# Performance work log

Hardware: AMD Instinct MI355X
Metric: run time of the kernel (lower is better)

## Reference

```python
import jax, jax.numpy as jnp
import numpy as np

B, N_FRAMES, C, S = 4, 32, 256, 16
D = 512            # attn_dim = min(C*S*S, 512)
NHEADS = 8
TOKEN = C * S * S  # 65536
EPS = 1e-5


def _layer_norm_last(x, g, b):
    mu = x.mean(-1, keepdims=True)
    var = x.var(-1, keepdims=True)
    return (x - mu) * jax.lax.rsqrt(var + EPS) * g + b


def _forward(feat, Wp, bp, Wu, bu, Wq, bq, Wk, bk, Wv, bv, Wo, bo, ln1_g, ln1_b,
             Wk1, bk1, Wk2, bk2, Wpc, bpc, gn_g, gn_b, Wf1, bf1, Wf2, bf2,
             dn_g, dn_b, num_frames):
    BN, Cc, H, W = feat.shape
    N = num_frames
    Bb = BN // N
    # 1) flatten frames to tokens and project (B, N, token_dim) -> (B, N, D)
    tokens = feat.reshape(Bb, N, Cc * H * W)
    tp = tokens @ Wp.T + bp
    # contextual grouping with clamped indices: K = v_{n-1}, Q = v_n, V = v_{n+1}
    idx = jnp.arange(N)
    v_prev = tp[:, jnp.maximum(idx - 1, 0)]
    v_next = tp[:, jnp.minimum(idx + 1, N - 1)]
    # 2) MHA with seq_len 1 for Q/K/V (degenerate softmax over a single key)
    dh = D // NHEADS
    q = (tp @ Wq.T + bq).reshape(Bb, N, NHEADS, dh)
    k = (v_prev @ Wk.T + bk).reshape(Bb, N, NHEADS, dh)
    v = (v_next @ Wv.T + bv).reshape(Bb, N, NHEADS, dh)
    scores = jnp.sum(q * k, axis=-1, keepdims=True) / jnp.sqrt(jnp.float32(dh))  # (B,N,h,1)
    wts = jax.nn.softmax(scores, axis=-1)  # identically 1.0 (single key)
    attn = (wts * v).reshape(Bb, N, D) @ Wo.T + bo
    enh = _layer_norm_last(attn + tp, ln1_g, ln1_b)
    # 3) unproject back to feature maps
    feat_attn = (enh @ Wu.T + bu).reshape(BN, Cc, H, W)
    # 4) DynamicConv: per-sample depthwise 3x3 kernels conditioned on GAP
    gap = feat_attn.mean((2, 3))                       # (BN, C)
    hid = jax.nn.relu(gap @ Wk1.T + bk1)
    kern = (hid @ Wk2.T + bk2).reshape(BN, Cc, 3, 3)   # per-sample, per-channel kernels
    xp = jnp.pad(feat_attn, ((0, 0), (0, 0), (1, 1), (1, 1)))
    out = jnp.zeros_like(feat_attn)
    for di in range(3):  # fixed 3x3 kernel taps
        for dj in range(3):
            out = out + kern[:, :, di, dj][:, :, None, None] * xp[:, :, di:di + H, dj:dj + W]
    # 1x1 proj conv
    out = jnp.einsum('nchw,dc->ndhw', out, Wpc) + bpc[:, None, None]
    # GroupNorm(min(32,C))
    G = min(32, Cc)
    og = out.reshape(BN, G, -1)
    mu = og.mean(-1, keepdims=True)
    var = og.var(-1, keepdims=True)
    out = ((og - mu) * jax.lax.rsqrt(var + EPS)).reshape(BN, Cc, H, W)
    feat_dc = out * gn_g[:, None, None] + gn_b[:, None, None]
    # 5) dc_fc (1x1 conv -> relu -> 1x1 conv) + residual, then LayerNorm([C,S,S])
    y = jax.nn.relu(jnp.einsum('nchw,dc->ndhw', feat_dc, Wf1) + bf1[:, None, None])
    y = jnp.einsum('nchw,dc->ndhw', y, Wf2) + bf2[:, None, None]
    z = y + feat_attn
    zf = z.reshape(BN, -1)
    mu = zf.mean(-1, keepdims=True)
    var = zf.var(-1, keepdims=True)
    zn = ((zf - mu) * jax.lax.rsqrt(var + EPS)).reshape(BN, Cc, H, W)
    return zn * dn_g + dn_b


def setup_inputs() -> dict:
    key = jax.random.key(0)
    ks = jax.random.split(key, 16)
    sc = 0.02
    inp = {
        'feat': jax.random.normal(ks[0], (B * N_FRAMES, C, S, S), jnp.float32),
        'Wp': jax.random.normal(ks[1], (D, TOKEN), jnp.float32) * sc,
        'bp': jnp.zeros((D,), jnp.float32),
        'Wu': jax.random.normal(ks[2], (TOKEN, D), jnp.float32) * sc,
        'bu': jnp.zeros((TOKEN,), jnp.float32),
        'Wq': jax.random.normal(ks[3], (D, D), jnp.float32) * sc,
        'bq': jnp.zeros((D,), jnp.float32),
        'Wk': jax.random.normal(ks[4], (D, D), jnp.float32) * sc,
        'bk': jnp.zeros((D,), jnp.float32),
        'Wv': jax.random.normal(ks[5], (D, D), jnp.float32) * sc,
        'bv': jnp.zeros((D,), jnp.float32),
        'Wo': jax.random.normal(ks[6], (D, D), jnp.float32) * sc,
        'bo': jnp.zeros((D,), jnp.float32),
        'ln1_g': jnp.ones((D,), jnp.float32),
        'ln1_b': jnp.zeros((D,), jnp.float32),
        'Wk1': jax.random.normal(ks[7], (C, C), jnp.float32) * sc,
        'bk1': jnp.zeros((C,), jnp.float32),
        'Wk2': jax.random.normal(ks[8], (C * 9, C), jnp.float32) * sc,
        'bk2': jnp.zeros((C * 9,), jnp.float32),
        'Wpc': jax.random.normal(ks[9], (C, C), jnp.float32) * sc,
        'bpc': jnp.zeros((C,), jnp.float32),
        'gn_g': jnp.ones((C,), jnp.float32),
        'gn_b': jnp.zeros((C,), jnp.float32),
        'Wf1': jax.random.normal(ks[10], (C, C), jnp.float32) * sc,
        'bf1': jnp.zeros((C,), jnp.float32),
        'Wf2': jax.random.normal(ks[11], (C, C), jnp.float32) * sc,
        'bf2': jnp.zeros((C,), jnp.float32),
        'dn_g': jnp.ones((C, S, S), jnp.float32),
        'dn_b': jnp.zeros((C, S, S), jnp.float32),
        'num_frames': N_FRAMES,
    }
    return inp


def reference(feat, Wp, bp, Wu, bu, Wq, bq, Wk, bk, Wv, bv, Wo, bo, ln1_g, ln1_b,
              Wk1, bk1, Wk2, bk2, Wpc, bpc, gn_g, gn_b, Wf1, bf1, Wf2, bf2,
              dn_g, dn_b, num_frames):
    return _forward(feat, Wp, bp, Wu, bu, Wq, bq, Wk, bk, Wv, bv, Wo, bo,
                    ln1_g, ln1_b, Wk1, bk1, Wk2, bk2, Wpc, bpc, gn_g, gn_b,
                    Wf1, bf1, Wf2, bf2, dn_g, dn_b, num_frames)
```

## Files before the change

kernel.cpp:

```cpp
#include <hip/hip_runtime.h>


typedef unsigned short u16;
typedef unsigned int u32;
typedef __attribute__((ext_vector_type(8))) short short8;
typedef __attribute__((ext_vector_type(4))) float floatx4;

__device__ __forceinline__ float b2f(u16 h){ return __uint_as_float(((u32)h)<<16); }
__device__ __forceinline__ u16 f2b(float f){
  u32 u = __float_as_uint(f);
  u = (u + 0x7FFFu + ((u>>16)&1u)) >> 16;
  return (u16)u;
}
__device__ __forceinline__ u32 cvtpk(float lo, float hi){
  u32 r;
  asm("v_cvt_pk_bf16_f32 %0, %1, %2" : "=v"(r) : "v"(lo), "v"(hi));
  return r;
}
__device__ __forceinline__ float blo(u32 w){ return __uint_as_float(w<<16); }
__device__ __forceinline__ float bhi(u32 w){ return __uint_as_float(w & 0xFFFF0000u); }
__device__ __forceinline__ bool probe_f32(const u32* p){ return p[0]==0x3F800000u; }

__device__ __forceinline__ void gload_lds16(const void* g, void* l){
  __builtin_amdgcn_global_load_lds(
      (const __attribute__((address_space(1))) unsigned int*)g,
      (__attribute__((address_space(3))) unsigned int*)l, 16, 0, 0);
}

__device__ __forceinline__ float wred(float v){
  #pragma unroll
  for (int o=32;o>0;o>>=1) v += __shfl_down(v, o, 64);
  return v;
}

__device__ __forceinline__ float dot8(uint4 u, const float* t){
  return t[0]*blo(u.x)+t[1]*bhi(u.x)+t[2]*blo(u.y)+t[3]*bhi(u.y)
       + t[4]*blo(u.z)+t[5]*bhi(u.z)+t[6]*blo(u.w)+t[7]*bhi(u.w);
}

__device__ __forceinline__ void bar_lgkm(){
  asm volatile("s_waitcnt lgkmcnt(0)" ::: "memory");
  __builtin_amdgcn_sched_barrier(0);
  __builtin_amdgcn_s_barrier();
  asm volatile("" ::: "memory");
}
__device__ __forceinline__ void bar(){
  asm volatile("" ::: "memory");
  __builtin_amdgcn_s_barrier();
  asm volatile("" ::: "memory");
}

struct SrcTab { const void* p[22]; };

__global__ __launch_bounds__(256) void cvt_k(SrcTab st, const u32* probe, u16* dst){
  constexpr int ns[22]   = {262144,262144,65536,589824,65536,65536,65536,65536,65536,
                            65536,512,512,512,512,512,256,2304,256,256,256,256,256};
  constexpr int offs[22] = {0,262144,524288,589824,1179648,1245184,1310720,1376256,1441792,
                            1507328,1572864,1573376,1573888,1574400,1574912,1575424,1575680,
                            1577984,1578240,1578496,1578752,1579008};
  int t = blockIdx.y;
  int e = (blockIdx.x*256 + threadIdx.x)*4;
  if (e >= ns[t]) return;
  u16* d = dst + offs[t] + e;
  if (probe_f32(probe)){
    float4 v = *(const float4*)((const float*)st.p[t] + e);
    d[0]=f2b(v.x); d[1]=f2b(v.y); d[2]=f2b(v.z); d[3]=f2b(v.w);
  } else {
    *(uint2*)d = *(const uint2*)((const u16*)st.p[t] + e);
  }
}

__global__ __launch_bounds__(256) void gemm32_k(
    const void* __restrict__ Ap, int lda,
    const void* __restrict__ Bp, int ldb,
    float* __restrict__ Cp, int N, int kchunk,
    const u32* __restrict__ probe)
{
  __shared__ __align__(16) char As0[8192];
  __shared__ __align__(16) char Bs0[8192];
  __shared__ __align__(16) char As1[8192];
  __shared__ __align__(16) char Bs1[8192];

  const bool pf32 = probe_f32(probe);
  const int tid = threadIdx.x;
  const int lane = tid & 63, wv = tid >> 6;
  const int mw = wv >> 1, nw = wv & 1;
  const int m0 = blockIdx.x * 64, n0 = blockIdx.y * 64;
  const int k0 = blockIdx.z * kchunk, kend = k0 + kchunk;

  floatx4 zf = {0.f,0.f,0.f,0.f};
  floatx4 acc[2][2];
  acc[0][0]=zf; acc[0][1]=zf; acc[1][0]=zf; acc[1][1]=zf;

  const int ml = lane & 15, q = lane >> 4;

  auto stage32 = [&](char* As, char* Bs, int kk){
    #pragma unroll
    for (int i=0;i<2;i++){
      int g = wv*2 + i;
      int ci = g*64 + lane;
      int row = ci >> 3, slot = ci & 7;
      int c = slot ^ (row & 7);
      gload_lds16((const float*)Ap + (size_t)(m0+row)*lda + kk + c*4, As + g*1024);
      gload_lds16((const float*)Bp + (size_t)(n0+row)*ldb + kk + c*4, Bs + g*1024);
    }
  };
  auto compute32 = [&](const char* As, const char* Bs){
    short8 af[2], bf2[2];
    #pragma unroll
    for (int i=0;i<2;i++){
      int arow = mw*32 + ml + i*16;
      int r7 = arow & 7;
      uint4 u0 = *(const uint4*)(As + arow*128 + ((q*2)   ^ r7)*16);
      uint4 u1 = *(const uint4*)(As + arow*128 + ((q*2+1) ^ r7)*16);
      uint4 t;
      t.x = cvtpk(__uint_as_float(u0.x), __uint_as_float(u0.y));
      t.y = cvtpk(__uint_as_float(u0.z), __uint_as_float(u0.w));
      t.z = cvtpk(__uint_as_float(u1.x), __uint_as_float(u1.y));
      t.w = cvtpk(__uint_as_float(u1.z), __uint_as_float(u1.w));
      union { uint4 u; short8 s; } ca; ca.u = t; af[i] = ca.s;
      int brow = nw*32 + ml + i*16;
      int s7 = brow & 7;
      uint4 v0 = *(const uint4*)(Bs + brow*128 + ((q*2)   ^ s7)*16);
      uint4 v1 = *(const uint4*)(Bs + brow*128 + ((q*2+1) ^ s7)*16);
      uint4 w4;
      w4.x = cvtpk(__uint_as_float(v0.x), __uint_as_float(v0.y));
      w4.y = cvtpk(__uint_as_float(v0.z), __uint_as_float(v0.w));
      w4.z = cvtpk(__uint_as_float(v1.x), __uint_as_float(v1.y));
      w4.w = cvtpk(__uint_as_float(v1.z), __uint_as_float(v1.w));
      union { uint4 u; short8 s; } cb; cb.u = w4; bf2[i] = cb.s;
    }
    acc[0][0] = __builtin_amdgcn_mfma_f32_16x16x32_bf16(af[0], bf2[0], acc[0][0], 0,0,0);
    acc[0][1] = __builtin_amdgcn_mfma_f32_16x16x32_bf16(af[0], bf2[1], acc[0][1], 0,0,0);
    acc[1][0] = __builtin_amdgcn_mfma_f32_16x16x32_bf16(af[1], bf2[0], acc[1][0], 0,0,0);
    acc[1][1] = __builtin_amdgcn_mfma_f32_16x16x32_bf16(af[1], bf2[1], acc[1][1], 0,0,0);
  };

  auto stage16 = [&](char* As, char* Bs, int kk){
    int ci = wv*64 + lane;
    int row = ci >> 2, slot = ci & 3;
    int c = slot ^ ((row>>1) & 3);
    gload_lds16((const u16*)Ap + (size_t)(m0+row)*lda + kk + c*8, As + wv*1024);
    gload_lds16((const u16*)Bp + (size_t)(n0+row)*ldb + kk + c*8, Bs + wv*1024);
  };
  auto compute16 = [&](const char* As, const char* Bs){
    short8 af[2], bf2[2];
    #pragma unroll
    for (int i=0;i<2;i++){
      int arow = mw*32 + ml + i*16;
      int sa = q ^ ((arow>>1) & 3);
      union { uint4 u; short8 s; } ca; ca.u = *(const uint4*)(As + arow*64 + sa*16);
      af[i] = ca.s;
      int brow = nw*32 + ml + i*16;
      int sb = q ^ ((brow>>1) & 3);
      union { uint4 u; short8 s; } cb; cb.u = *(const uint4*)(Bs + brow*64 + sb*16);
      bf2[i] = cb.s;
    }
    acc[0][0] = __builtin_amdgcn_mfma_f32_16x16x32_bf16(af[0], bf2[0], acc[0][0], 0,0,0);
    acc[0][1] = __builtin_amdgcn_mfma_f32_16x16x32_bf16(af[0], bf2[1], acc[0][1], 0,0,0);
    acc[1][0] = __builtin_amdgcn_mfma_f32_16x16x32_bf16(af[1], bf2[0], acc[1][0], 0,0,0);
    acc[1][1] = __builtin_amdgcn_mfma_f32_16x16x32_bf16(af[1], bf2[1], acc[1][1], 0,0,0);
  };

  if (pf32){
    stage32(As0, Bs0, k0);
    __syncthreads();
    for (int kk = k0; kk < kend; kk += 64){
      stage32(As1, Bs1, kk + 32);
      compute32(As0, Bs0);
      __syncthreads();
      if (kk + 64 < kend) stage32(As0, Bs0, kk + 64);
      compute32(As1, Bs1);
      __syncthreads();
    }
  } else {
    stage16(As0, Bs0, k0);
    __syncthreads();
    for (int kk = k0; kk < kend; kk += 64){
      stage16(As1, Bs1, kk + 32);
      compute16(As0, Bs0);
      __syncthreads();
      if (kk + 64 < kend) stage16(As0, Bs0, kk + 64);
      compute16(As1, Bs1);
      __syncthreads();
    }
  }

  const int colg = lane & 15, quad = lane >> 4;
  #pragma unroll
  for (int mi=0;mi<2;mi++){
    #pragma unroll
    for (int ni=0;ni<2;ni++){
      #pragma unroll
      for (int r=0;r<4;r++){
        int m = m0 + mw*32 + mi*16 + quad*4 + r;
        int n = n0 + nw*32 + ni*16 + colg;
        atomicAdd(&Cp[(size_t)m*N + n], acc[mi][ni][r]);
      }
    }
  }
}

template<int MODE>
__global__ __launch_bounds__(256) void gemm_k(
    const void* __restrict__ Ap, int lda,
    const void* __restrict__ Bp, int ldb,
    void* __restrict__ Cp, int N, int Ktot, int kchunk,
    const u16* __restrict__ bias,
    const float* __restrict__ gnst,
    const u16* __restrict__ gng, const u16* __restrict__ gnb,
    const u16* __restrict__ fres,
    const u32* __restrict__ probe, int araw, int braw)
{
  __shared__ __align__(16) u16 As[64*72];
  __shared__ __align__(16) u16 Bs[64*72];

  const bool pf32 = probe_f32(probe);
  const bool a32 = araw && pf32, b32 = braw && pf32;

  const int tid = threadIdx.x;
  const int lane = tid & 63, wv = tid >> 6;
  const int mw = wv >> 1, nw = wv & 1;
  const int m0 = blockIdx.x * 64, n0 = blockIdx.y * 64;
  int k0 = 0, kend = Ktot;
  (void)kchunk;

  floatx4 zf = {0.f,0.f,0.f,0.f};
  floatx4 acc[2][2];
  acc[0][0]=zf; acc[0][1]=zf; acc[1][0]=zf; acc[1][1]=zf;

  const int ml = lane & 15, q = lane >> 4;
  const int ar0 = (mw*32 + ml)*72 + q*8;
  const int ar1 = ar0 + 16*72;
  const int br0 = (nw*32 + ml)*72 + q*8;
  const int br1 = br0 + 16*72;

  const int row0 = tid >> 3, colc = tid & 7;

  auto ld_tiles = [&](uint4 (&pa)[2][2], uint4 (&pb)[2][2], int kk){
    #pragma unroll
    for (int i=0;i<2;i++){
      int row = row0 + i*32;
      if (a32){
        const float* s = (const float*)Ap + (size_t)(m0+row)*lda + kk + colc*8;
        pa[i][0] = ((const uint4*)s)[0];
        pa[i][1] = ((const uint4*)s)[1];
      } else {
        const u16* s = (const u16*)Ap + (size_t)(m0+row)*lda + kk + colc*8;
        pa[i][0] = *(const uint4*)s;
      }
      if (b32){
        const float* s = (const float*)Bp + (size_t)(n0+row)*ldb + kk + colc*8;
        pb[i][0] = ((const uint4*)s)[0];
        pb[i][1] = ((const uint4*)s)[1];
      } else {
        const u16* s = (const u16*)Bp + (size_t)(n0+row)*ldb + kk + colc*8;
        pb[i][0] = *(const uint4*)s;
      }
    }
  };

  auto stage = [&](uint4 (&pa)[2][2], uint4 (&pb)[2][2], int kk){
    #pragma unroll
    for (int i=0;i<2;i++){
      int row = row0 + i*32;
      u16* adst = &As[row*72 + colc*8];
      if (MODE == 3){
        uint4 u = pa[i][0];
        int nsamp = (m0+row) >> 8;
        int cbase = kk + colc*8;
        int g = cbase >> 3;
        float mu = gnst[(nsamp*32+g)*2], rs = gnst[(nsamp*32+g)*2+1];
        float f[8] = {blo(u.x),bhi(u.x),blo(u.y),bhi(u.y),blo(u.z),bhi(u.z),blo(u.w),bhi(u.w)};
        float fn[8];
        #pragma unroll
        for (int j=0;j<8;j++){
          int c = cbase + j;
          fn[j] = (f[j]-mu)*rs*b2f(gng[c]) + b2f(gnb[c]);
        }
        uint4 t4;
        t4.x = cvtpk(fn[0],fn[1]); t4.y = cvtpk(fn[2],fn[3]);
        t4.z = cvtpk(fn[4],fn[5]); t4.w = cvtpk(fn[6],fn[7]);
        *(uint4*)adst = t4;
      } else if (a32){
        uint4 v0 = pa[i][0], v1 = pa[i][1];
        uint4 t4;
        t4.x = cvtpk(__uint_as_float(v0.x), __uint_as_float(v0.y));
        t4.y = cvtpk(__uint_as_float(v0.z), __uint_as_float(v0.w));
        t4.z = cvtpk(__uint_as_float(v1.x), __uint_as_float(v1.y));
        t4.w = cvtpk(__uint_as_float(v1.z), __uint_as_float(v1.w));
        *(uint4*)adst = t4;
      } else {
        *(uint4*)adst = pa[i][0];
      }
      u16* bdst = &Bs[row*72 + colc*8];
      if (b32){
        uint4 v0 = pb[i][0], v1 = pb[i][1];
        uint4 t4;
        t4.x = cvtpk(__uint_as_float(v0.x), __uint_as_float(v0.y));
        t4.y = cvtpk(__uint_as_float(v0.z), __uint_as_float(v0.w));
        t4.z = cvtpk(__uint_as_float(v1.x), __uint_as_float(v1.y));
        t4.w = cvtpk(__uint_as_float(v1.z), __uint_as_float(v1.w));
        *(uint4*)bdst = t4;
      } else {
        *(uint4*)bdst = pb[i][0];
      }
    }
  };

  auto mfma_step = [&](){
    #pragma unroll
    for (int ks2=0; ks2<2; ks2++){
      int ko = ks2*32;
      short8 a0 = *(const short8*)&As[ar0 + ko];
      short8 a1 = *(const short8*)&As[ar1 + ko];
      short8 b0 = *(const short8*)&Bs[br0 + ko];
      short8 b1 = *(const short8*)&Bs[br1 + ko];
      acc[0][0] = __builtin_amdgcn_mfma_f32_16x16x32_bf16(a0, b0, acc[0][0], 0,0,0);
      acc[0][1] = __builtin_amdgcn_mfma_f32_16x16x32_bf16(a0, b1, acc[0][1], 0,0,0);
      acc[1][0] = __builtin_amdgcn_mfma_f32_16x16x32_bf16(a1, b0, acc[1][0], 0,0,0);
      acc[1][1] = __builtin_amdgcn_mfma_f32_16x16x32_bf16(a1, b1, acc[1][1], 0,0,0);
    }
  };

  uint4 pa0[2][2], pb0[2][2], pa1[2][2], pb1[2][2];
  ld_tiles(pa0, pb0, k0);
  for (int kk = k0; kk < kend; kk += 128){
    bar();
    ld_tiles(pa1, pb1, kk + 64);
    stage(pa0, pb0, kk);
    bar_lgkm();
    mfma_step();
    bar();
    if (kk + 128 < kend) ld_tiles(pa0, pb0, kk + 128);
    stage(pa1, pb1, kk + 64);
    bar_lgkm();
    mfma_step();
  }

  const int colg = lane & 15, quad = lane >> 4;
  #pragma unroll
  for (int mi=0;mi<2;mi++){
    #pragma unroll
    for (int ni=0;ni<2;ni++){
      #pragma unroll
      for (int r=0;r<4;r++){
        int m = m0 + mw*32 + mi*16 + quad*4 + r;
        int n = n0 + nw*32 + ni*16 + colg;
        float v = acc[mi][ni][r];
        if (MODE==1){
          ((u16*)Cp)[(size_t)m*N + n] = f2b(v + b2f(bias[n]));
        } else if (MODE==3){
          ((u16*)Cp)[(size_t)m*N + n] = f2b(fmaxf(v + b2f(bias[n]), 0.f));
        } else if (MODE==4){
          int nsp = m >> 8, s = m & 255;
          ((u16*)Cp)[(size_t)m*N + n] =
              f2b(v + b2f(bias[n]) + b2f(fres[(size_t)nsp*65536 + (size_t)n*256 + s]));
        }
      }
    }
  }
}

__global__ __launch_bounds__(512) void attn_ln_k(
    const float* __restrict__ tp, const u16* __restrict__ Wv, const u16* __restrict__ bv,
    const u16* __restrict__ Wo, const u16* __restrict__ bo, const u16* __restrict__ bp,
    const u16* __restrict__ g, const u16* __restrict__ bln, u16* __restrict__ enh)
{
  __shared__ float tpr[512], tpn[512], vv[512], red[16];
  int r = blockIdx.x; int n = r & 31; int rn = (n==31) ? r : r+1;
  int t = threadIdx.x;
  float bpv = b2f(bp[t]);
  tpr[t] = tp[(size_t)r*512 + t] + bpv;
  tpn[t] = tp[(size_t)rn*512 + t] + bpv;
  __syncthreads();
  {
    const uint4* w4 = (const uint4*)(Wv + (size_t)t*512);
    float acc = b2f(bv[t]);
    #pragma unroll 8
    for (int i=0;i<64;i++) acc += dot8(w4[i], &tpn[i*8]);
    vv[t] = acc;
  }
  __syncthreads();
  float x;
  {
    const uint4* w4 = (const uint4*)(Wo + (size_t)t*512);
    float acc = b2f(bo[t]);
    #pragma unroll 8
    for (int i=0;i<64;i++) acc += dot8(w4[i], &vv[i*8]);
    x = acc + tpr[t];
  }
  float s1 = wred(x), s2 = wred(x*x);
  int lane = t & 63, wid = t >> 6;
  if (lane==0){ red[wid] = s1; red[8+wid] = s2; }
  __syncthreads();
  if (t==0){
    float a=0.f, b=0.f;
    #pragma unroll
    for (int i=0;i<8;i++){ a += red[i]; b += red[8+i]; }
    float mu = a/512.f; float var = b/512.f - mu*mu;
    red[0]=mu; red[1]=rsqrtf(var+1e-5f);
  }
  __syncthreads();
  float mu = red[0], rs = red[1];
  enh[(size_t)r*512 + t] = f2b((x-mu)*rs*b2f(g[t]) + b2f(bln[t]));
}

__global__ __launch_bounds__(256) void gap_k(const u16* __restrict__ fa, float* __restrict__ gapb){
  int wid = threadIdx.x>>6, lane = threadIdx.x&63;
  int pair = blockIdx.x*4 + wid;
  const uint2* p = (const uint2*)(fa + (size_t)pair*256);
  uint2 v = p[lane];
  float s = wred(blo(v.x)+bhi(v.x)+blo(v.y)+bhi(v.y));
  if (lane==0) gapb[pair] = s * (1.0f/256.0f);
}

__global__ __launch_bounds__(256) void hidkern_k(
    const float* __restrict__ gapb, const u16* __restrict__ Wk1, const u16* __restrict__ bk1,
    const u16* __restrict__ Wk2, const u16* __restrict__ bk2, float* __restrict__ kernb)
{
  __shared__ float gl[256], hl[256];
  int nn = blockIdx.x, t = threadIdx.x;
  gl[t] = gapb[(size_t)nn*256 + t];
  __syncthreads();
  {
    const uint4* w4 = (const uint4*)(Wk1 + (size_t)t*256);
    float acc = b2f(bk1[t]);
    #pragma unroll 8
    for (int i=0;i<32;i++) acc += dot8(w4[i], &gl[i*8]);
    hl[t] = fmaxf(acc, 0.f);
  }
  __syncthreads();
  for (int qq=0; qq<9; qq++){
    int e = t*9 + qq;
    const uint4* w4 = (const uint4*)(Wk2 + (size_t)e*256);
    float acc = b2f(bk2[e]);
    #pragma unroll 8
    for (int i=0;i<32;i++) acc += dot8(w4[i], &hl[i*8]);
    kernb[(size_t)nn*2304 + e] = acc;
  }
}

__global__ __launch_bounds__(256) void conv_k(
    const u16* __restrict__ fa, const float* __restrict__ kernb, u16* __restrict__ dwb)
{
  int b = blockIdx.x; int h = b & 15; int nn = b >> 4; int c = threadIdx.x;
  float kv[9];
  #pragma unroll
  for (int qq=0; qq<9; qq++) kv[qq] = kernb[(size_t)nn*2304 + c*9 + qq];
  float rowv[3][18];
  #pragma unroll
  for (int di=0; di<3; di++){
    int hh = h + di - 1;
    if (hh >= 0 && hh < 16){
      const u16* rp = fa + (size_t)nn*65536 + (size_t)c*256 + hh*16;
      rowv[di][0] = 0.f; rowv[di][17] = 0.f;
      #pragma unroll
      for (int w=0; w<16; w++) rowv[di][w+1] = b2f(rp[w]);
    } else {
      #pragma unroll
      for (int x=0; x<18; x++) rowv[di][x] = 0.f;
    }
  }
  #pragma unroll
  for (int w=0; w<16; w++){
    float o = 0.f;
    #pragma unroll
    for (int di=0; di<3; di++)
      o += kv[di*3]*rowv[di][w] + kv[di*3+1]*rowv[di][w+1] + kv[di*3+2]*rowv[di][w+2];
    dwb[((size_t)nn*256 + h*16 + w)*256 + c] = f2b(o);
  }
}

__global__ __launch_bounds__(256) void gnstats_k(const u16* __restrict__ out2, float* __restrict__ gnst){
  int wid = threadIdx.x>>6, lane = threadIdx.x&63;
  int grp = blockIdx.x*4 + wid; int nn = grp >> 5; int gg = grp & 31;
  const u16* base = out2 + (size_t)nn*65536 + gg*8;
  float s=0.f, ss=0.f;
  #pragma unroll 4
  for (int i=0;i<32;i++){
    int f = i*64 + lane; int sidx = f >> 3; int j = f & 7;
    float v = b2f(base[(size_t)sidx*256 + j]);
    s += v; ss += v*v;
  }
  s = wred(s); ss = wred(ss);
  if (lane==0){
    float mu = s/2048.f; float var = ss/2048.f - mu*mu;
    gnst[grp*2] = mu; gnst[grp*2+1] = rsqrtf(var + 1e-5f);
  }
}

__global__ __launch_bounds__(256) void lnstats_k(const u16* __restrict__ z, float* __restrict__ lnst){
  __shared__ float red[8];
  int nn = blockIdx.x, t = threadIdx.x;
  const uint4* p = (const uint4*)(z + (size_t)nn*65536);
  float s=0.f, ss=0.f;
  for (int i=0;i<32;i++){
    uint4 v = p[(size_t)i*256 + t];
    float f0=blo(v.x),f1=bhi(v.x),f2=blo(v.y),f3=bhi(v.y);
    float f4=blo(v.z),f5=bhi(v.z),f6=blo(v.w),f7=bhi(v.w);
    s  += (f0+f1)+(f2+f3)+(f4+f5)+(f6+f7);
    ss += (f0*f0+f1*f1)+(f2*f2+f3*f3)+(f4*f4+f5*f5)+(f6*f6+f7*f7);
  }
  s = wred(s); ss = wred(ss);
  int lane = t&63, wid = t>>6;
  if (lane==0){ red[wid]=s; red[4+wid]=ss; }
  __syncthreads();
  if (t==0){
    float a=red[0]+red[1]+red[2]+red[3];
    float b=red[4]+red[5]+red[6]+red[7];
    float mu = a/65536.f; float var = b/65536.f - mu*mu;
    lnst[nn*2] = mu; lnst[nn*2+1] = rsqrtf(var + 1e-5f);
  }
}

__global__ __launch_bounds__(256) void final_k(
    const u16* __restrict__ z, const float* __restrict__ lnst,
    const u16* __restrict__ dng, const u16* __restrict__ dnb,
    void* __restrict__ outp, const u32* __restrict__ probe)
{
  __shared__ float zt[32*257];
  const bool pf32 = probe_f32(probe);
  int b = blockIdx.x; int nn = b >> 3; int s0 = (b & 7)*32;
  int t = threadIdx.x;
  {
    int srow = t >> 3; int c0 = (t & 7)*32;
    const uint4* p = (const uint4*)(z + (size_t)nn*65536 + (size_t)(s0+srow)*256 + c0);
    float* dst = &zt[srow*257 + c0];
    #pragma unroll
    for (int i=0;i<4;i++){
      uint4 v = p[i];
      dst[i*8+0]=blo(v.x); dst[i*8+1]=bhi(v.x); dst[i*8+2]=blo(v.y); dst[i*8+3]=bhi(v.y);
      dst[i*8+4]=blo(v.z); dst[i*8+5]=bhi(v.z); dst[i*8+6]=blo(v.w); dst[i*8+7]=bhi(v.w);
    }
  }
  __syncthreads();
  float mu = lnst[nn*2], rs = lnst[nn*2+1];
  int sl = t & 31, cq = t >> 5;
  for (int i=0;i<32;i++){
    int c = i*8 + cq;
    float v = (zt[sl*257 + c] - mu) * rs;
    int gidx = c*256 + s0 + sl;
    float res = v*b2f(dng[gidx]) + b2f(dnb[gidx]);
    size_t oi = (size_t)nn*65536 + gidx;
    if (pf32) ((float*)outp)[oi] = res;
    else      ((u16*)outp)[oi]   = f2b(res);
  }
}

extern "C" void kernel_launch(void* const* d_in, const int* in_sizes, int n_in,
                              void* d_out, int out_size, void* d_ws, size_t ws_size,
                              hipStream_t stream) {
  (void)in_sizes; (void)n_in; (void)out_size; (void)ws_size;
  const u32* probe = (const u32*)d_in[21];

  char* w = (char*)d_ws;
  u16* cvt = (u16*)w;
  u16 *cWv  = cvt+0,       *cWo  = cvt+262144, *cWk1 = cvt+524288, *cWk2 = cvt+589824;
  u16 *cWpc = cvt+1179648, *cWf1 = cvt+1245184,*cWf2 = cvt+1310720;
  u16 *cdng = cvt+1376256, *cdnb = cvt+1441792,*cbu  = cvt+1507328;
  u16 *cbp  = cvt+1572864, *cbv  = cvt+1573376,*cbo  = cvt+1573888;
  u16 *cln1g= cvt+1574400, *cln1b= cvt+1574912,*cbk1 = cvt+1575424,*cbk2 = cvt+1575680;
  u16 *cbpc = cvt+1577984, *cgng = cvt+1578240,*cgnb = cvt+1578496;
  u16 *cbf1 = cvt+1578752, *cbf2 = cvt+1579008;

  float* tp_raw = (float*)(w + 4194304);
  u16*   enh    = (u16*)  (w + 4456448);
  float* gapb   = (float*)(w + 4587520);
  float* kernb  = (float*)(w + 4718592);
  float* gnst   = (float*)(w + 5898240);
  float* lnst   = (float*)(w + 5931008);
  u16*   fa     = (u16*)  (w + 8388608);
  u16*   out2   = (u16*)  (w + 25165824);
  u16*   z      = out2;
  u16*   dwb    = (u16*)d_out;
  u16*   y1     = dwb;

  SrcTab st;
  st.p[0]=d_in[9];  st.p[1]=d_in[11]; st.p[2]=d_in[15]; st.p[3]=d_in[17];
  st.p[4]=d_in[19]; st.p[5]=d_in[23]; st.p[6]=d_in[25]; st.p[7]=d_in[27];
  st.p[8]=d_in[28]; st.p[9]=d_in[4];  st.p[10]=d_in[2]; st.p[11]=d_in[10];
  st.p[12]=d_in[12];st.p[13]=d_in[13];st.p[14]=d_in[14];st.p[15]=d_in[16];
  st.p[16]=d_in[18];st.p[17]=d_in[20];st.p[18]=d_in[21];st.p[19]=d_in[22];
  st.p[20]=d_in[24];st.p[21]=d_in[26];

  cvt_k<<<dim3(576,22), 256, 0, stream>>>(st, probe, cvt);
  hipMemsetAsync(tp_raw, 0, 128*512*4, stream);
  gemm32_k<<<dim3(2,8,64), 256, 0, stream>>>(d_in[0], 65536, d_in[1], 65536, tp_raw,
      512, 1024, probe);
  attn_ln_k<<<128, 512, 0, stream>>>(tp_raw, cWv, cbv, cWo, cbo, cbp, cln1g, cln1b, enh);
  gemm_k<1><<<dim3(2,1024,1), 256, 0, stream>>>(enh, 512, d_in[3], 512, fa,
      65536, 512, 0, cbu, nullptr, nullptr, nullptr, nullptr, probe, 0, 1);
  gap_k<<<8192, 256, 0, stream>>>(fa, gapb);
  hidkern_k<<<128, 256, 0, stream>>>(gapb, cWk1, cbk1, cWk2, cbk2, kernb);
  conv_k<<<2048, 256, 0, stream>>>(fa, kernb, dwb);
  gemm_k<1><<<dim3(512,4,1), 256, 0, stream>>>(dwb, 256, cWpc, 256, out2,
      256, 256, 0, cbpc, nullptr, nullptr, nullptr, nullptr, probe, 0, 0);
  gnstats_k<<<1024, 256, 0, stream>>>(out2, gnst);
  gemm_k<3><<<dim3(512,4,1), 256, 0, stream>>>(out2, 256, cWf1, 256, y1,
      256, 256, 0, cbf1, gnst, cgng, cgnb, nullptr, probe, 0, 0);
  gemm_k<4><<<dim3(512,4,1), 256, 0, stream>>>(y1, 256, cWf2, 256, z,
      256, 256, 0, cbf2, nullptr, nullptr, nullptr, fa, probe, 0, 0);
  lnstats_k<<<128, 256, 0, stream>>>(z, lnst);
  final_k<<<1024, 256, 0, stream>>>(z, lnst, cdng, cdnb, d_out, probe);
}
```

Before: 615.7 us.

## Triple-buffer split-K projection GEMM with vmcnt waits and XCD-aware block mapping

The split-K token-projection GEMM moves from double buffering with full __syncthreads to a three-stage LDS ring. Each stage waits only on the older global-to-LDS loads (partial vmcnt) before a single barrier, so two loads stay in flight while a stage computes. The grid becomes 1D and is remapped so the 16 output tiles of one K-chunk share an XCD, which should improve L2 reuse of the A/B slices. The cost is more LDS per block, 48KB, which may lower occupancy, and correctness now depends on getting the vmcnt counts exactly right.

```diff
diff --git a/kernel.cpp b/kernel.cpp
--- a/kernel.cpp
+++ b/kernel.cpp
@@ -46,6 +46,24 @@
 }
 __device__ __forceinline__ void bar(){
   asm volatile("" ::: "memory");
+  __builtin_amdgcn_s_barrier();
+  asm volatile("" ::: "memory");
+}
+__device__ __forceinline__ void bar_vm4(){
+  asm volatile("s_waitcnt vmcnt(4)" ::: "memory");
+  __builtin_amdgcn_sched_barrier(0);
+  __builtin_amdgcn_s_barrier();
+  asm volatile("" ::: "memory");
+}
+__device__ __forceinline__ void bar_vm2(){
+  asm volatile("s_waitcnt vmcnt(2)" ::: "memory");
+  __builtin_amdgcn_sched_barrier(0);
+  __builtin_amdgcn_s_barrier();
+  asm volatile("" ::: "memory");
+}
+__device__ __forceinline__ void bar_vm0(){
+  asm volatile("s_waitcnt vmcnt(0)" ::: "memory");
+  __builtin_amdgcn_sched_barrier(0);
   __builtin_amdgcn_s_barrier();
   asm volatile("" ::: "memory");
 }
@@ -76,17 +94,20 @@
     float* __restrict__ Cp, int N, int kchunk,
     const u32* __restrict__ probe)
 {
-  __shared__ __align__(16) char As0[8192];
-  __shared__ __align__(16) char Bs0[8192];
-  __shared__ __align__(16) char As1[8192];
-  __shared__ __align__(16) char Bs1[8192];
+  __shared__ __align__(16) char sm[3][16384];
 
   const bool pf32 = probe_f32(probe);
   const int tid = threadIdx.x;
   const int lane = tid & 63, wv = tid >> 6;
   const int mw = wv >> 1, nw = wv & 1;
-  const int m0 = blockIdx.x * 64, n0 = blockIdx.y * 64;
-  const int k0 = blockIdx.z * kchunk, kend = k0 + kchunk;
+
+  const int bid = blockIdx.x;
+  const int xcd = bid & 7, slot = bid >> 3;
+  const int chunk = (slot >> 4)*8 + xcd;
+  const int within = slot & 15;
+  const int m0 = (within & 1) * 64, n0 = (within >> 1) * 64;
+  const int k0 = chunk * kchunk;
+  const int P = kchunk >> 5;
 
   floatx4 zf = {0.f,0.f,0.f,0.f};
   floatx4 acc[2][2];
@@ -94,18 +115,20 @@
 
   const int ml = lane & 15, q = lane >> 4;
 
-  auto stage32 = [&](char* As, char* Bs, int kk){
+  auto stage32 = [&](char* buf, int kk){
+    char* As = buf; char* Bs = buf + 8192;
     #pragma unroll
     for (int i=0;i<2;i++){
       int g = wv*2 + i;
       int ci = g*64 + lane;
-      int row = ci >> 3, slot = ci & 7;
-      int c = slot ^ (row & 7);
+      int row = ci >> 3, sl = ci & 7;
+      int c = sl ^ (row & 7);
       gload_lds16((const float*)Ap + (size_t)(m0+row)*lda + kk + c*4, As + g*1024);
       gload_lds16((const float*)Bp + (size_t)(n0+row)*ldb + kk + c*4, Bs + g*1024);
     }
   };
-  auto compute32 = [&](const char* As, const char* Bs){
+  auto compute32 = [&](const char* buf){
+    const char* As = buf; const char* Bs = buf + 8192;
     short8 af[2], bf2[2];
     #pragma unroll
     for (int i=0;i<2;i++){
@@ -136,14 +159,16 @@
     acc[1][1] = __builtin_amdgcn_mfma_f32_16x16x32_bf16(af[1], bf2[1], acc[1][1], 0,0,0);
   };
 
-  auto stage16 = [&](char* As, char* Bs, int kk){
+  auto stage16 = [&](char* buf, int kk){
+    char* As = buf; char* Bs = buf + 4096;
     int ci = wv*64 + lane;
-    int row = ci >> 2, slot = ci & 3;
-    int c = slot ^ ((row>>1) & 3);
+    int row = ci >> 2, sl = ci & 3;
+    int c = sl ^ ((row>>1) & 3);
     gload_lds16((const u16*)Ap + (size_t)(m0+row)*lda + kk + c*8, As + wv*1024);
     gload_lds16((const u16*)Bp + (size_t)(n0+row)*ldb + kk + c*8, Bs + wv*1024);
   };
-  auto compute16 = [&](const char* As, const char* Bs){
+  auto compute16 = [&](const char* buf){
+    const char* As = buf; const char* Bs = buf + 4096;
     short8 af[2], bf2[2];
     #pragma unroll
     for (int i=0;i<2;i++){
@@ -163,27 +188,27 @@
   };
 
   if (pf32){
-    stage32(As0, Bs0, k0);
-    __syncthreads();
-    for (int kk = k0; kk < kend; kk += 64){
-      stage32(As1, Bs1, kk + 32);
-      compute32(As0, Bs0);
-      __syncthreads();
-      if (kk + 64 < kend) stage32(As0, Bs0, kk + 64);
-      compute32(As1, Bs1);
-      __syncthreads();
-    }
+    stage32(sm[0], k0);
+    stage32(sm[1], k0 + 32);
+    int p = 0;
+    for (; p < P-2; ++p){
+      bar_vm4();
+      stage32(sm[(p+2)%3], k0 + 32*(p+2));
+      compute32(sm[p%3]);
+    }
+    bar_vm4();  compute32(sm[p%3]); ++p;
+    bar_vm0();  compute32(sm[p%3]);
   } else {
-    stage16(As0, Bs0, k0);
-    __syncthreads();
-    for (int kk = k0; kk < kend; kk += 64){
-      stage16(As1, Bs1, kk + 32);
-      compute16(As0, Bs0);
-      __syncthreads();
-      if (kk + 64 < kend) stage16(As0, Bs0, kk + 64);
-      compute16(As1, Bs1);
-      __syncthreads();
-    }
+    stage16(sm[0], k0);
+    stage16(sm[1], k0 + 32);
+    int p = 0;
+    for (; p < P-2; ++p){
+      bar_vm2();
+      stage16(sm[(p+2)%3], k0 + 32*(p+2));
+      compute16(sm[p%3]);
+    }
+    bar_vm2();  compute16(sm[p%3]); ++p;
+    bar_vm0();  compute16(sm[p%3]);
   }
 
   const int colg = lane & 15, quad = lane >> 4;
@@ -586,7 +611,7 @@
 
   cvt_k<<<dim3(576,22), 256, 0, stream>>>(st, probe, cvt);
   hipMemsetAsync(tp_raw, 0, 128*512*4, stream);
-  gemm32_k<<<dim3(2,8,64), 256, 0, stream>>>(d_in[0], 65536, d_in[1], 65536, tp_raw,
+  gemm32_k<<<1024, 256, 0, stream>>>(d_in[0], 65536, d_in[1], 65536, tp_raw,
       512, 1024, probe);
   attn_ln_k<<<128, 512, 0, stream>>>(tp_raw, cWv, cbv, cWo, cbo, cbp, cln1g, cln1b, enh);
   gemm_k<1><<<dim3(2,1024,1), 256, 0, stream>>>(enh, 512, d_in[3], 512, fa,
```

After: 633.5 us. +2.9%, slower.
